# Performance work log

Measured on AMD Instinct MI355X. Metric: run time of the kernel, lower is better.

## Reference

```python
import jax, jax.numpy as jnp
import numpy as np

B, N, HN, HE, H = 8, 128, 256, 128, 8
DH = HN // H
P = N * (N - 1) // 2


def _ln(x, g, b, eps=1e-5):
    m = jnp.mean(x, axis=-1, keepdims=True)
    v = jnp.mean((x - m) ** 2, axis=-1, keepdims=True)
    return (x - m) * jax.lax.rsqrt(v + eps) * g + b


def setup_inputs() -> dict:
    key = jax.random.key(0)
    ks = jax.random.split(key, 16)
    i1, i2 = np.triu_indices(N, k=1)  # all unordered pairs, P = N(N-1)/2
    s = lambda fan: 1.0 / np.sqrt(fan)
    return {
        "node_feat": jax.random.normal(ks[0], (B, N, HN), jnp.float32),
        "edge_feat": jax.random.normal(ks[1], (B, P, HE), jnp.float32),
        "x_idx1": jnp.asarray(i1, jnp.int32),
        "x_idx2": jnp.asarray(i2, jnp.int32),
        "mask_valid": jax.random.bernoulli(ks[2], 0.9, (B, P)).astype(jnp.float32),
        "Wqkv": jax.random.normal(ks[3], (HN, 3 * HN), jnp.float32) * s(HN),
        "bqkv": jnp.zeros((3 * HN,), jnp.float32),
        "Wev": jax.random.normal(ks[4], (HE, HN), jnp.float32) * s(HE),
        "bev": jnp.zeros((HN,), jnp.float32),
        "Wea": jax.random.normal(ks[5], (HE, H), jnp.float32) * s(HE),
        "bea": jnp.zeros((H,), jnp.float32),
        "Wo": jax.random.normal(ks[6], (2 * HN, HN), jnp.float32) * s(2 * HN),
        "bo": jnp.zeros((HN,), jnp.float32),
        "Wsk": jax.random.normal(ks[7], (HN, 2 * HN), jnp.float32) * s(HN),
        "bsk": jnp.zeros((2 * HN,), jnp.float32),
        "gn": jnp.ones((HN,), jnp.float32),
        "bn": jnp.zeros((HN,), jnp.float32),
        "ge": jnp.ones((HE,), jnp.float32),
        "be": jnp.zeros((HE,), jnp.float32),
    }


def reference(node_feat, edge_feat, x_idx1, x_idx2, mask_valid,
              Wqkv, bqkv, Wev, bev, Wea, bea, Wo, bo, Wsk, bsk,
              gn, bn, ge, be):
    n_in = _ln(node_feat, gn, bn)                      # [B,N,HN]
    e_in = _ln(edge_feat, ge, be)                      # [B,P,HE]
    q, k, v = jnp.split(n_in @ Wqkv + bqkv, 3, axis=-1)
    to_h = lambda t: t.reshape(B, -1, H, DH).transpose(0, 2, 1, 3)
    q, k, v = to_h(q), to_h(k), to_h(v)                # [B,H,N,DH]
    e_val = to_h(e_in @ Wev + bev)                     # [B,H,P,DH]
    e_adj = (e_in @ Wea + bea).transpose(0, 2, 1)      # [B,H,P]

    scale = DH ** -0.5
    logits = jnp.einsum('bhqd,bhkd->bhqk', q, k) * scale  # [B,H,N,N]
    # per-pair logits; torch stacks [qk, edge_adj] then sums -> just add
    l_node1 = logits[:, :, x_idx1, x_idx2] + e_adj     # node i1 attends to i2
    l_node2 = logits[:, :, x_idx2, x_idx1] + e_adj     # node i2 attends to i1
    v_node1 = e_val + v[:, :, x_idx2]                  # value node i1 receives
    v_node2 = e_val + v[:, :, x_idx1]

    # group the 2P directed edges by destination node (= torch cat+sort+reshape)
    cat_idx = jnp.concatenate([x_idx1, x_idx2])        # [2P]
    order = jnp.argsort(cat_idx)                       # stable sort
    gl = jnp.concatenate([l_node1, l_node2], axis=2)[:, :, order].reshape(B, H, N, N - 1)
    gv = jnp.concatenate([v_node1, v_node2], axis=2)[:, :, order].reshape(B, H, N, N - 1, DH)
    gm = jnp.concatenate([mask_valid, mask_valid], axis=1)[:, order].reshape(B, N, N - 1)[:, None]  # [B,1,N,N-1]

    gl = jnp.where(gm == 0.0, -9e15, gl)
    probs = jax.nn.softmax(gl, axis=3)
    probs = probs * jnp.any(gm != 0.0, axis=3, keepdims=True).astype(probs.dtype)
    attn = jnp.einsum('bhnk,bhnkd->bhnd', probs, gv)   # [B,H,N,DH]
    attn = attn.transpose(0, 2, 1, 3).reshape(B, N, HN)

    comb = jax.nn.gelu(jnp.concatenate([n_in, attn], axis=-1) @ Wo + bo, approximate=False)
    val, gate = jnp.split(comb @ Wsk + bsk, 2, axis=-1)
    g = jax.nn.sigmoid(gate)
    return node_feat * (1.0 - g) + val * g
```

## Files before the change

kernel.cpp:

```cpp
#include <hip/hip_runtime.h>
#include <hip/hip_bf16.h>
#include <math.h>

#define BB 8
#define NN 128
#define HN 256
#define HE 128
#define NH 8
#define DH 32
#define PP 8128
#define BP (BB*PP)

typedef __hip_bfloat16 bf16;
typedef __hip_bfloat162 bf162;
typedef __attribute__((ext_vector_type(8))) short bf16x8;
typedef __attribute__((ext_vector_type(4))) float f32x4;

__device__ __forceinline__ float bf2f(bf16 x){ return __bfloat162float(x); }
__device__ __forceinline__ float bfraw2f(short u){
  return __uint_as_float(((unsigned)(unsigned short)u) << 16);
}

__device__ __forceinline__ float wave_sum(float v){
  #pragma unroll
  for (int off=32; off>=1; off>>=1) v += __shfl_xor(v, off, 64);
  return v;
}
__device__ __forceinline__ float wave_max(float v){
  #pragma unroll
  for (int off=32; off>=1; off>>=1) v = fmaxf(v, __shfl_xor(v, off, 64));
  return v;
}
__device__ __forceinline__ float g16_sum(float v){
  #pragma unroll
  for (int off=8; off>=1; off>>=1) v += __shfl_xor(v, off, 16);
  return v;
}

__device__ __forceinline__ int pair_idx(int a, int c){
  int i = a < c ? a : c;
  int j = a < c ? c : a;
  return ((i*(255 - i))>>1) + (j - i - 1);
}

#define C_NODE 0LL
#define C_MASK 262144LL
#define C_WQKV 327168LL
#define C_BQKV 523776LL
#define C_WEV  524544LL
#define C_BEV  557312LL
#define C_WEA  557568LL
#define C_BEA  558592LL
#define C_WO   558600LL
#define C_BO   689672LL
#define C_WSK  689928LL
#define C_BSK  821000LL
#define C_GN   821512LL
#define C_BN   821768LL
#define C_GE   822024LL
#define C_BE   822152LL
#define IOFF   822400LL
#define TOT8   102785
#define CONVBLKS 402
#define I_NIN  0LL
#define I_Q    262144LL
#define I_K    524288LL
#define I_V    786432LL
#define I_ATTN 1048576LL
#define I_COMB 1310720LL
#define I_EA2  1572864LL
#define I_XG   2093056LL
#define I_EVAL 6254592LL
#define I_WT   14577664LL
#define I_WOB  14594048LL
#define I_WSKB 14659584LL
#define I_FLG  14725120LL

struct SrcPtrs { const void* p[16]; };

__global__ __launch_bounds__(256) void k_convert(SrcPtrs sp, float* __restrict__ dst,
                                                 int* __restrict__ flags,
                                                 const unsigned short* __restrict__ nodeRaw,
                                                 const void* __restrict__ rawWev,
                                                 bf16* __restrict__ Wt,
                                                 const void* __restrict__ rawWo,
                                                 const void* __restrict__ rawWsk,
                                                 bf16* __restrict__ WoB,
                                                 bf16* __restrict__ WskB)
{
  __shared__ int sbad;
  if (threadIdx.x == 0) sbad = 0;
  __syncthreads();
  {
    int bad = 0;
    for (int i = threadIdx.x; i < 1024; i += 256){
      unsigned e = (nodeRaw[i] >> 7) & 0xFFu;
      if (e >= 194u) bad = 1;
    }
    if (bad) sbad = 1;
  }
  __syncthreads();
  const int f32 = sbad;
  if (blockIdx.x == 0 && threadIdx.x == 0) flags[0] = f32;

  if (blockIdx.x >= CONVBLKS + 128){
    int o = (blockIdx.x - (CONVBLKS + 128))*256 + threadIdx.x;
    const void* src = (o < 16384) ? rawWo : rawWsk;
    bf16* dw = (o < 16384) ? WoB : WskB;
    int lo = (o < 16384) ? o : o - 16384;
    if (f32){
      const float4* s4 = (const float4*)src;
      float4 a0 = s4[2*lo], a1 = s4[2*lo+1];
      union { float4 f; bf16 h[8]; } cv;
      cv.h[0]=__float2bfloat16(a0.x); cv.h[1]=__float2bfloat16(a0.y);
      cv.h[2]=__float2bfloat16(a0.z); cv.h[3]=__float2bfloat16(a0.w);
      cv.h[4]=__float2bfloat16(a1.x); cv.h[5]=__float2bfloat16(a1.y);
      cv.h[6]=__float2bfloat16(a1.z); cv.h[7]=__float2bfloat16(a1.w);
      *reinterpret_cast<float4*>(dw + lo*8) = cv.f;
    } else {
      *reinterpret_cast<float4*>(dw + lo*8) = ((const float4*)src)[lo];
    }
    return;
  }

  if (blockIdx.x >= CONVBLKS){
    int idx = (blockIdx.x - CONVBLKS)*256 + threadIdx.x;
    float v = f32 ? ((const float*)rawWev)[idx]
                  : bfraw2f(((const short*)rawWev)[idx]);
    Wt[(idx & 255)*128 + (idx >> 8)] = __float2bfloat16(v);
    return;
  }

  int o = blockIdx.x*256 + threadIdx.x;
  if (o >= TOT8) return;
  const int cum[17] = {0,32768,40896,65472,65568,69664,69696,69824,69825,
                       86209,86241,102625,102689,102721,102753,102769,102785};
  int s = 0;
  #pragma unroll
  for (int i = 1; i <= 15; i++) if (o >= cum[i]) s = i;
  const int li = o - cum[s];
  float4 r0, r1;
  if (f32){
    const float4* src = (const float4*)sp.p[s];
    r0 = src[2*li]; r1 = src[2*li+1];
  } else {
    union { float4 f; unsigned short u[8]; } cv;
    cv.f = ((const float4*)sp.p[s])[li];
    r0.x = __uint_as_float((unsigned)cv.u[0] << 16);
    r0.y = __uint_as_float((unsigned)cv.u[1] << 16);
    r0.z = __uint_as_float((unsigned)cv.u[2] << 16);
    r0.w = __uint_as_float((unsigned)cv.u[3] << 16);
    r1.x = __uint_as_float((unsigned)cv.u[4] << 16);
    r1.y = __uint_as_float((unsigned)cv.u[5] << 16);
    r1.z = __uint_as_float((unsigned)cv.u[6] << 16);
    r1.w = __uint_as_float((unsigned)cv.u[7] << 16);
  }
  float4* d = (float4*)(dst + (long long)cum[s]*8);
  d[2*li]   = r0;
  d[2*li+1] = r1;
}

__global__ __launch_bounds__(256) void k1_node_ln_qkv(
    const float* __restrict__ cnode, const float* __restrict__ cWqkv,
    const float* __restrict__ cbqkv, const float* __restrict__ cgn, const float* __restrict__ cbn,
    float* __restrict__ nin_ws, float* __restrict__ q_ws, float* __restrict__ k_ws,
    float* __restrict__ v_ws)
{
  __shared__ float xln[4][HN];
  const int t = threadIdx.x, wv = t>>6, lane = t&63;
  const int cb = blockIdx.x % 3;
  const int g0 = (blockIdx.x / 3) * 4;
  {
    int g = g0 + wv;
    float x[4];
    #pragma unroll
    for (int i=0;i<4;i++) x[i] = cnode[g*HN + lane + 64*i];
    float s = x[0]+x[1]+x[2]+x[3];
    s = wave_sum(s);
    float m = s * (1.0f/HN);
    float q = 0.f;
    #pragma unroll
    for (int i=0;i<4;i++){ float d = x[i]-m; q += d*d; }
    q = wave_sum(q);
    float rstd = rsqrtf(fmaxf(q*(1.0f/HN), 0.f) + 1e-5f);
    #pragma unroll
    for (int i=0;i<4;i++){
      int c = lane + 64*i;
      float y = (x[i]-m)*rstd*cgn[c] + cbn[c];
      xln[wv][c] = y;
      if (cb == 0) nin_ws[g*HN + c] = y;
    }
  }
  __syncthreads();
  const int col = cb*256 + t;
  float acc[4];
  {
    float bb = cbqkv[col];
    #pragma unroll
    for (int r=0;r<4;r++) acc[r] = bb;
  }
  for (int k=0;k<HN;k+=4){
    float4 xv[4];
    #pragma unroll
    for (int r=0;r<4;r++) xv[r] = *reinterpret_cast<const float4*>(&xln[r][k]);
    #pragma unroll
    for (int kk=0;kk<4;kk++){
      float w = cWqkv[(k+kk)*768 + col];
      #pragma unroll
      for (int r=0;r<4;r++) acc[r] = fmaf((&xv[r].x)[kk], w, acc[r]);
    }
  }
  float* dstp = (cb == 0) ? q_ws : (cb == 1) ? k_ws : v_ws;
  const int h = t>>5, d = t&31;
  #pragma unroll
  for (int r=0;r<4;r++){
    int g = g0 + r;
    int b = g>>7, n = g&127;
    dstp[((b*NH + h)*NN + n)*DH + d] = acc[r];
  }
}

__global__ __launch_bounds__(256) void k2a_edge_ln(
    const void* __restrict__ edge_raw, const float* __restrict__ cWea,
    const float* __restrict__ cbea, const float* __restrict__ cge,
    const float* __restrict__ cbe, const float* __restrict__ cmask,
    bf16* __restrict__ xg, float* __restrict__ ea2, const int* __restrict__ flags)
{
  __shared__ float xlnS[16][136];
  __shared__ float part[128];
  const int t = threadIdx.x;
  const int R0 = blockIdx.x*16;
  const int b = R0 / PP;
  const int p0 = R0 - b*PP;
  const int f32 = flags[0];
  {
    int r = t>>4, sub = t&15;
    long base = (long)(R0 + r)*HE + sub*8;
    float x[8];
    if (f32){
      const float* cef = (const float*)edge_raw + base;
      float4 a0 = *reinterpret_cast<const float4*>(cef);
      float4 a1 = *reinterpret_cast<const float4*>(cef + 4);
      x[0]=a0.x; x[1]=a0.y; x[2]=a0.z; x[3]=a0.w;
      x[4]=a1.x; x[5]=a1.y; x[6]=a1.z; x[7]=a1.w;
    } else {
      union { float4 f; short u[8]; } cv;
      cv.f = *reinterpret_cast<const float4*>((const bf16*)edge_raw + base);
      #pragma unroll
      for (int i=0;i<8;i++) x[i] = bfraw2f(cv.u[i]);
    }
    float s = 0.f;
    #pragma unroll
    for (int i=0;i<8;i++) s += x[i];
    s = g16_sum(s);
    float m = s*(1.0f/HE);
    float q = 0.f;
    #pragma unroll
    for (int i=0;i<8;i++){ float dd = x[i]-m; q += dd*dd; }
    q = g16_sum(q);
    float rstd = rsqrtf(fmaxf(q*(1.0f/HE), 0.f) + 1e-5f);
    #pragma unroll
    for (int i=0;i<8;i++){
      int c = sub*8 + i;
      xlnS[r][c] = (x[i]-m)*rstd*cge[c] + cbe[c];
    }
  }
  __syncthreads();
  {
    int r = t>>4, c0 = (t&15)*8;
    union { float4 f; bf16 h[8]; } o;
    #pragma unroll
    for (int i=0;i<8;i++) o.h[i] = __float2bfloat16(xlnS[r][c0+i]);
    *reinterpret_cast<float4*>(xg + (long)(R0 + r)*HE + c0) = o.f;
  }
  {
    const int c = t & 7, r = (t>>3) & 15, half = t>>7;
    const int pid = r*8 + c;
    float s = half ? 0.0f : cbea[c];
    const int k0 = half*64;
    #pragma unroll 8
    for (int k=k0; k<k0+64; k++) s = fmaf(xlnS[r][k], cWea[k*NH + c], s);
    if (half){ part[pid] = s; }
    __syncthreads();
    if (!half){
      s += part[pid];
      int p = p0 + r;
      float mk = cmask[b*PP + p];
      ea2[(b*NH + c)*PP + p] = (mk != 0.0f) ? s : -9e15f;
    }
  }
}

__global__ __launch_bounds__(256) void k2b_mfma(
    const bf16* __restrict__ xg, const bf16* __restrict__ Wt,
    const float* __restrict__ cbev, bf16* __restrict__ e_val)
{
  __shared__ bf16 Xs[64][136];
  __shared__ bf16 Ws[64][136];
  const int t = threadIdx.x;
  const int rowblk = blockIdx.x >> 2;
  const int cb = blockIdx.x & 3;
  const int b = rowblk / 127;
  const int p0 = (rowblk - b*127) * 64;
  const int n0 = cb * 64;
  #pragma unroll
  for (int it = 0; it < 4; ++it){
    int idx = it*256 + t;
    int r = idx >> 4, seg = idx & 15;
    float4 xv = *reinterpret_cast<const float4*>(xg + (long)(b*PP + p0 + r)*HE + seg*8);
    *reinterpret_cast<float4*>(&Xs[r][seg*8]) = xv;
    float4 wv = *reinterpret_cast<const float4*>(Wt + (long)(n0 + r)*HE + seg*8);
    *reinterpret_cast<float4*>(&Ws[r][seg*8]) = wv;
  }
  __syncthreads();
  const int wv = t>>6, lane = t&63;
  const int fm = lane & 15, q = lane >> 4;
  f32x4 acc[4];
  #pragma unroll
  for (int ct=0; ct<4; ++ct){
    float bb = cbev[n0 + ct*16 + fm];
    acc[ct][0]=bb; acc[ct][1]=bb; acc[ct][2]=bb; acc[ct][3]=bb;
  }
  #pragma unroll
  for (int ks=0; ks<4; ++ks){
    bf16x8 A = *reinterpret_cast<const bf16x8*>(&Xs[wv*16 + fm][ks*32 + q*8]);
    #pragma unroll
    for (int ct=0; ct<4; ++ct){
      bf16x8 Bf = *reinterpret_cast<const bf16x8*>(&Ws[ct*16 + fm][ks*32 + q*8]);
      acc[ct] = __builtin_amdgcn_mfma_f32_16x16x32_bf16(A, Bf, acc[ct], 0, 0, 0);
    }
  }
  #pragma unroll
  for (int ct=0; ct<4; ++ct){
    int col = n0 + ct*16 + fm;
    int h = col >> 5, d = col & 31;
    #pragma unroll
    for (int reg=0; reg<4; ++reg){
      int p = p0 + wv*16 + q*4 + reg;
      e_val[((long)(b*NH + h)*PP + p)*DH + d] = __float2bfloat16(acc[ct][reg]);
    }
  }
}

__global__ __launch_bounds__(256) void k3_attn(
    const float* __restrict__ q_ws, const float* __restrict__ k_ws, const float* __restrict__ v_ws,
    const bf16* __restrict__ e_val, const float* __restrict__ ea2,
    float* __restrict__ attn)
{
  __shared__ float kT[DH][NN+1];
  __shared__ float vS[NN][DH+1];
  __shared__ float qS[8][DH];
  __shared__ float pbuf[4][NN];
  const int t = threadIdx.x, wv = t>>6, lane = t&63;
  const int s16 = blockIdx.x & 15, h = (blockIdx.x>>4)&7, b = blockIdx.x>>7;
  const int bh = b*NH + h;
  const int n0 = s16*8;
  const float* kb = k_ws + (long)bh*NN*DH;
  const float* vb = v_ws + (long)bh*NN*DH;
  const float* qb = q_ws + ((long)bh*NN + n0)*DH;
  for (int idx=t; idx<NN*DH; idx+=256){
    int m = idx>>5, d = idx&31;
    kT[d][m] = kb[idx];
    vS[m][d] = vb[idx];
  }
  if (t < 8*DH) reinterpret_cast<float*>(qS)[t] = qb[t];
  __syncthreads();
  const float scale = 0.17677669529663687f;
  const float* eab = ea2 + (long)bh*PP;
  const bf16* evp = e_val + (long)bh*PP*DH;
  for (int it=0; it<2; ++it){
    const int nn = it*4 + wv;
    const int n = n0 + nn;
    const int m1 = lane, m2 = lane + 64;
    float dot1 = 0.f, dot2 = 0.f;
    #pragma unroll
    for (int d=0; d<DH; d++){
      float qd = qS[nn][d];
      dot1 = fmaf(qd, kT[d][m1], dot1);
      dot2 = fmaf(qd, kT[d][m2], dot2);
    }
    const bool self1 = (m1 == n), self2 = (m2 == n);
    int pr1 = pair_idx(n, self1 ? (m1^1) : m1);
    int pr2 = pair_idx(n, self2 ? (m2^1) : m2);
    float ea1 = eab[pr1], ea2v = eab[pr2];
    float l1 = self1 ? -INFINITY : dot1*scale + ea1;
    float l2 = self2 ? -INFINITY : dot2*scale + ea2v;
    bool av = (!self1 && ea1 > -8.9e15f) || (!self2 && ea2v > -8.9e15f);
    float lm = wave_max(fmaxf(l1, l2));
    float e1 = __expf(l1 - lm), e2 = __expf(l2 - lm);
    float ssum = wave_sum(e1 + e2);
    int anyv = __any((int)av);
    float inv = anyv ? (1.0f/ssum) : 0.0f;
    pbuf[wv][m1] = e1*inv;
    pbuf[wv][m2] = e2*inv;
    const int msub = lane & 15, oct = lane >> 4;
    float acc[8];
    #pragma unroll
    for (int e=0;e<8;e++) acc[e] = 0.f;
    #pragma unroll
    for (int mm=0; mm<128; mm+=16){
      int m = mm + msub;
      int ms = (m==n) ? (m^1) : m;
      int pr = pair_idx(n, ms);
      bf16x8 ev8 = *reinterpret_cast<const bf16x8*>(evp + (long)pr*DH + oct*8);
      float pm = pbuf[wv][m];
      const float* vrow = &vS[m][oct*8];
      #pragma unroll
      for (int e=0;e<8;e++){
        acc[e] = fmaf(pm, vrow[e] + bfraw2f(ev8[e]), acc[e]);
      }
    }
    #pragma unroll
    for (int off=1; off<16; off<<=1){
      #pragma unroll
      for (int e=0;e<8;e++) acc[e] += __shfl_xor(acc[e], off, 64);
    }
    if (msub == 0){
      float* op = attn + ((long)b*NN + n)*HN + h*DH + oct*8;
      float4 o0 = {acc[0],acc[1],acc[2],acc[3]};
      float4 o1 = {acc[4],acc[5],acc[6],acc[7]};
      *reinterpret_cast<float4*>(op) = o0;
      *reinterpret_cast<float4*>(op+4) = o1;
    }
  }
}

__global__ __launch_bounds__(256) void k4_wo_gelu(
    const float* __restrict__ nin_ws, const float* __restrict__ attn,
    const bf16* __restrict__ WoB, const float* __restrict__ cbo,
    float* __restrict__ comb)
{
  __shared__ float xc[4][512];
  __shared__ float ps[3][4][64];
  const int t = threadIdx.x;
  const int g0 = (blockIdx.x >> 2) * 4;
  const int cq = blockIdx.x & 3;
  {
    int r = t>>6, c0 = (t&63)*8;
    const float* src = (c0 < 256) ? (nin_ws + (long)(g0+r)*HN + c0)
                                  : (attn + (long)(g0+r)*HN + (c0-256));
    float4 a0 = *reinterpret_cast<const float4*>(src);
    float4 a1 = *reinterpret_cast<const float4*>(src+4);
    *reinterpret_cast<float4*>(&xc[r][c0]) = a0;
    *reinterpret_cast<float4*>(&xc[r][c0+4]) = a1;
  }
  __syncthreads();
  const int cidx = t & 63, ks = t >> 6;
  const int col = cq*64 + cidx;
  float acc[4] = {0.f,0.f,0.f,0.f};
  const int k0 = ks*128;
  #pragma unroll 4
  for (int k=k0; k<k0+128; k++){
    float w = bf2f(WoB[k*HN + col]);
    #pragma unroll
    for (int r=0;r<4;r++) acc[r] = fmaf(xc[r][k], w, acc[r]);
  }
  if (ks){
    #pragma unroll
    for (int r=0;r<4;r++) ps[ks-1][r][cidx] = acc[r];
  }
  __syncthreads();
  if (!ks){
    float bb = cbo[col];
    #pragma unroll
    for (int r=0;r<4;r++){
      float x = acc[r] + bb + ps[0][r][cidx] + ps[1][r][cidx] + ps[2][r][cidx];
      comb[(long)(g0+r)*HN + col] = 0.5f*x*(1.0f + erff(x*0.7071067811865475f));
    }
  }
}

__global__ __launch_bounds__(256) void k5_sk_gate(
    const float* __restrict__ comb, const float* __restrict__ cnode,
    const bf16* __restrict__ WskB, const float* __restrict__ cbsk,
    void* __restrict__ out, const int* __restrict__ flags)
{
  __shared__ float xc[4][HN];
  __shared__ float psv[3][4][64];
  __shared__ float psg[3][4][64];
  const int t = threadIdx.x;
  const int g0 = (blockIdx.x >> 2) * 4;
  const int cq = blockIdx.x & 3;
  {
    int r = t>>6, c0 = (t&63)*4;
    *reinterpret_cast<float4*>(&xc[r][c0]) =
        *reinterpret_cast<const float4*>(comb + (long)(g0+r)*HN + c0);
  }
  __syncthreads();
  const int cidx = t & 63, ks = t >> 6;
  const int col = cq*64 + cidx;
  float av[4] = {0.f,0.f,0.f,0.f}, ag[4] = {0.f,0.f,0.f,0.f};
  const int k0 = ks*64;
  #pragma unroll 4
  for (int k=k0; k<k0+64; k++){
    float wv = bf2f(WskB[k*512 + col]);
    float wg = bf2f(WskB[k*512 + col + 256]);
    #pragma unroll
    for (int r=0;r<4;r++){
      float xr = xc[r][k];
      av[r] = fmaf(xr, wv, av[r]);
      ag[r] = fmaf(xr, wg, ag[r]);
    }
  }
  if (ks){
    #pragma unroll
    for (int r=0;r<4;r++){ psv[ks-1][r][cidx] = av[r]; psg[ks-1][r][cidx] = ag[r]; }
  }
  __syncthreads();
  if (!ks){
    const int f32 = flags[0];
    float bv = cbsk[col], bg = cbsk[col+256];
    #pragma unroll
    for (int r=0;r<4;r++){
      float v = av[r] + bv + psv[0][r][cidx] + psv[1][r][cidx] + psv[2][r][cidx];
      float g = ag[r] + bg + psg[0][r][cidx] + psg[1][r][cidx] + psg[2][r][cidx];
      float gg = 1.0f/(1.0f + __expf(-g));
      float nf = cnode[(long)(g0+r)*HN + col];
      float res = nf*(1.0f - gg) + v*gg;
      if (f32) ((float*)out)[(long)(g0+r)*HN + col] = res;
      else ((bf16*)out)[(long)(g0+r)*HN + col] = __float2bfloat16(res);
    }
  }
}

extern "C" void kernel_launch(void* const* d_in, const int* in_sizes, int n_inputs,
                              void* d_out, int out_size, void* d_ws, size_t ws_size,
                              hipStream_t stream)
{
  float* ws = (float*)d_ws;
  float* c_node = ws + C_NODE;
  float* c_mask = ws + C_MASK;
  float* c_Wqkv = ws + C_WQKV;
  float* c_bqkv = ws + C_BQKV;
  float* c_bev  = ws + C_BEV;
  float* c_Wea  = ws + C_WEA;
  float* c_bea  = ws + C_BEA;
  float* c_bo   = ws + C_BO;
  float* c_bsk  = ws + C_BSK;
  float* c_gn   = ws + C_GN;
  float* c_bn   = ws + C_BN;
  float* c_ge   = ws + C_GE;
  float* c_be   = ws + C_BE;
  float* base   = ws + IOFF;
  float* nin_ws  = base + I_NIN;
  float* q_ws    = base + I_Q;
  float* k_ws    = base + I_K;
  float* v_ws    = base + I_V;
  float* attn_ws = base + I_ATTN;
  float* comb_ws = base + I_COMB;
  float* ea2_ws  = base + I_EA2;
  bf16*  xg_ws   = (bf16*)(base + I_XG);
  bf16*  eval_ws = (bf16*)(base + I_EVAL);
  bf16*  wt_ws   = (bf16*)(base + I_WT);
  bf16*  wob_ws  = (bf16*)(base + I_WOB);
  bf16*  wskb_ws = (bf16*)(base + I_WSKB);
  int*   flags   = (int*)(base + I_FLG);

  SrcPtrs sp;
  sp.p[0]  = d_in[0];
  sp.p[1]  = d_in[4];
  sp.p[2]  = d_in[5];
  sp.p[3]  = d_in[6];
  sp.p[4]  = d_in[7];
  sp.p[5]  = d_in[8];
  sp.p[6]  = d_in[9];
  sp.p[7]  = d_in[10];
  sp.p[8]  = d_in[11];
  sp.p[9]  = d_in[12];
  sp.p[10] = d_in[13];
  sp.p[11] = d_in[14];
  sp.p[12] = d_in[15];
  sp.p[13] = d_in[16];
  sp.p[14] = d_in[17];
  sp.p[15] = d_in[18];

  k_convert<<<CONVBLKS + 256, 256, 0, stream>>>(sp, ws, flags,
                                                (const unsigned short*)d_in[0],
                                                d_in[7], wt_ws,
                                                d_in[11], d_in[13],
                                                wob_ws, wskb_ws);
  k1_node_ln_qkv<<<768, 256, 0, stream>>>(c_node, c_Wqkv, c_bqkv, c_gn, c_bn,
                                          nin_ws, q_ws, k_ws, v_ws);
  k2a_edge_ln<<<BP/16, 256, 0, stream>>>(d_in[1], c_Wea, c_bea, c_ge, c_be, c_mask,
                                         xg_ws, ea2_ws, flags);
  k2b_mfma<<<4064, 256, 0, stream>>>(xg_ws, wt_ws, c_bev, eval_ws);
  k3_attn<<<BB*NH*16, 256, 0, stream>>>(q_ws, k_ws, v_ws, eval_ws, ea2_ws, attn_ws);
  k4_wo_gelu<<<1024, 256, 0, stream>>>(nin_ws, attn_ws, wob_ws, c_bo, comb_ws);
  k5_sk_gate<<<1024, 256, 0, stream>>>(comb_ws, c_node, wskb_ws, c_bsk, d_out, flags);
}
```

Before: 200.2 us.

## Fold edge-value projection after attention aggregation, dropping e_val materialization

Removes the separate MFMA kernel that computed and stored per-pair edge values (B*H*P*DH bf16). Because the projection is linear, the attention kernel now aggregates the normalized edge features with the attention probabilities and then applies Wev once per node and head, adding the bias scaled by the any-valid flag. Attention is reorganized to one block per (batch, node) covering all heads, with ea2 and v re-laid out so the per-pair reads are contiguous. This cuts a large intermediate write and read. In exchange each block gathers 128 rows of edge features and each thread runs a small scalar GEMV.

Result: slower. 238.0 us (+18.9%).

```diff
diff --git a/kernel.cpp b/kernel.cpp
--- a/kernel.cpp
+++ b/kernel.cpp
@@ -24,11 +24,6 @@
 __device__ __forceinline__ float wave_sum(float v){
   #pragma unroll
   for (int off=32; off>=1; off>>=1) v += __shfl_xor(v, off, 64);
-  return v;
-}
-__device__ __forceinline__ float wave_max(float v){
-  #pragma unroll
-  for (int off=32; off>=1; off>>=1) v = fmaxf(v, __shfl_xor(v, off, 64));
   return v;
 }
 __device__ __forceinline__ float g16_sum(float v){
@@ -70,7 +65,6 @@
 #define I_COMB 1310720LL
 #define I_EA2  1572864LL
 #define I_XG   2093056LL
-#define I_EVAL 6254592LL
 #define I_WT   14577664LL
 #define I_WOB  14594048LL
 #define I_WSKB 14659584LL
@@ -210,13 +204,18 @@
       for (int r=0;r<4;r++) acc[r] = fmaf((&xv[r].x)[kk], w, acc[r]);
     }
   }
-  float* dstp = (cb == 0) ? q_ws : (cb == 1) ? k_ws : v_ws;
-  const int h = t>>5, d = t&31;
-  #pragma unroll
-  for (int r=0;r<4;r++){
-    int g = g0 + r;
-    int b = g>>7, n = g&127;
-    dstp[((b*NH + h)*NN + n)*DH + d] = acc[r];
+  if (cb == 2){
+    #pragma unroll
+    for (int r=0;r<4;r++) v_ws[(long)(g0+r)*HN + t] = acc[r];
+  } else {
+    float* dstp = (cb == 0) ? q_ws : k_ws;
+    const int h = t>>5, d = t&31;
+    #pragma unroll
+    for (int r=0;r<4;r++){
+      int g = g0 + r;
+      int b = g>>7, n = g&127;
+      dstp[((b*NH + h)*NN + n)*DH + d] = acc[r];
+    }
   }
 }
 
@@ -286,143 +285,134 @@
       s += part[pid];
       int p = p0 + r;
       float mk = cmask[b*PP + p];
-      ea2[(b*NH + c)*PP + p] = (mk != 0.0f) ? s : -9e15f;
-    }
-  }
-}
-
-__global__ __launch_bounds__(256) void k2b_mfma(
-    const bf16* __restrict__ xg, const bf16* __restrict__ Wt,
-    const float* __restrict__ cbev, bf16* __restrict__ e_val)
-{
-  __shared__ bf16 Xs[64][136];
-  __shared__ bf16 Ws[64][136];
+      ea2[((long)b*PP + p)*8 + c] = (mk != 0.0f) ? s : -9e15f;
+    }
+  }
+}
+
+__global__ __launch_bounds__(256) void k3_attn(
+    const float* __restrict__ q_ws,
+    const float* __restrict__ k_ws,
+    const float* __restrict__ v_ws,
+    const bf16* __restrict__ xg,
+    const float* __restrict__ ea2,
+    const bf16* __restrict__ Wt,
+    const float* __restrict__ cbev,
+    float* __restrict__ attn)
+{
+  __shared__ __align__(16) float qS[8][32];
+  __shared__ __align__(16) int   prS[128];
+  __shared__ __align__(16) float eaS[128][8];
+  __shared__ __align__(16) float pS[8][128];
+  __shared__ __align__(16) float sS[8][128];
+  __shared__ float anyS[8];
   const int t = threadIdx.x;
-  const int rowblk = blockIdx.x >> 2;
-  const int cb = blockIdx.x & 3;
-  const int b = rowblk / 127;
-  const int p0 = (rowblk - b*127) * 64;
-  const int n0 = cb * 64;
-  #pragma unroll
-  for (int it = 0; it < 4; ++it){
-    int idx = it*256 + t;
-    int r = idx >> 4, seg = idx & 15;
-    float4 xv = *reinterpret_cast<const float4*>(xg + (long)(b*PP + p0 + r)*HE + seg*8);
-    *reinterpret_cast<float4*>(&Xs[r][seg*8]) = xv;
-    float4 wv = *reinterpret_cast<const float4*>(Wt + (long)(n0 + r)*HE + seg*8);
-    *reinterpret_cast<float4*>(&Ws[r][seg*8]) = wv;
-  }
-  __syncthreads();
-  const int wv = t>>6, lane = t&63;
-  const int fm = lane & 15, q = lane >> 4;
-  f32x4 acc[4];
-  #pragma unroll
-  for (int ct=0; ct<4; ++ct){
-    float bb = cbev[n0 + ct*16 + fm];
-    acc[ct][0]=bb; acc[ct][1]=bb; acc[ct][2]=bb; acc[ct][3]=bb;
-  }
-  #pragma unroll
-  for (int ks=0; ks<4; ++ks){
-    bf16x8 A = *reinterpret_cast<const bf16x8*>(&Xs[wv*16 + fm][ks*32 + q*8]);
-    #pragma unroll
-    for (int ct=0; ct<4; ++ct){
-      bf16x8 Bf = *reinterpret_cast<const bf16x8*>(&Ws[ct*16 + fm][ks*32 + q*8]);
-      acc[ct] = __builtin_amdgcn_mfma_f32_16x16x32_bf16(A, Bf, acc[ct], 0, 0, 0);
-    }
-  }
-  #pragma unroll
-  for (int ct=0; ct<4; ++ct){
-    int col = n0 + ct*16 + fm;
-    int h = col >> 5, d = col & 31;
-    #pragma unroll
-    for (int reg=0; reg<4; ++reg){
-      int p = p0 + wv*16 + q*4 + reg;
-      e_val[((long)(b*NH + h)*PP + p)*DH + d] = __float2bfloat16(acc[ct][reg]);
-    }
-  }
-}
-
-__global__ __launch_bounds__(256) void k3_attn(
-    const float* __restrict__ q_ws, const float* __restrict__ k_ws, const float* __restrict__ v_ws,
-    const bf16* __restrict__ e_val, const float* __restrict__ ea2,
-    float* __restrict__ attn)
-{
-  __shared__ float kT[DH][NN+1];
-  __shared__ float vS[NN][DH+1];
-  __shared__ float qS[8][DH];
-  __shared__ float pbuf[4][NN];
-  const int t = threadIdx.x, wv = t>>6, lane = t&63;
-  const int s16 = blockIdx.x & 15, h = (blockIdx.x>>4)&7, b = blockIdx.x>>7;
-  const int bh = b*NH + h;
-  const int n0 = s16*8;
-  const float* kb = k_ws + (long)bh*NN*DH;
-  const float* vb = v_ws + (long)bh*NN*DH;
-  const float* qb = q_ws + ((long)bh*NN + n0)*DH;
-  for (int idx=t; idx<NN*DH; idx+=256){
-    int m = idx>>5, d = idx&31;
-    kT[d][m] = kb[idx];
-    vS[m][d] = vb[idx];
-  }
-  if (t < 8*DH) reinterpret_cast<float*>(qS)[t] = qb[t];
-  __syncthreads();
+  const int bid = blockIdx.x;
+  const int swz = (bid & 7)*128 + (bid >> 3);
+  const int n = swz & 127, b = swz >> 7;
+  const int h = t >> 5, ln = t & 31;
+
+  qS[h][ln] = q_ws[(((long)b*NH + h)*NN + n)*DH + ln];
+  if (t < 128){
+    int m = t;
+    prS[m] = pair_idx(n, (m == n) ? (m ^ 1) : m);
+  }
+  __syncthreads();
+  {
+    int m = t >> 1, c0 = (t & 1)*4;
+    float4 ev = *reinterpret_cast<const float4*>(ea2 + ((long)b*PP + prS[m])*8 + c0);
+    *reinterpret_cast<float4*>(&eaS[m][c0]) = ev;
+  }
+  __syncthreads();
+
   const float scale = 0.17677669529663687f;
-  const float* eab = ea2 + (long)bh*PP;
-  const bf16* evp = e_val + (long)bh*PP*DH;
-  for (int it=0; it<2; ++it){
-    const int nn = it*4 + wv;
-    const int n = n0 + nn;
-    const int m1 = lane, m2 = lane + 64;
-    float dot1 = 0.f, dot2 = 0.f;
-    #pragma unroll
-    for (int d=0; d<DH; d++){
-      float qd = qS[nn][d];
-      dot1 = fmaf(qd, kT[d][m1], dot1);
-      dot2 = fmaf(qd, kT[d][m2], dot2);
-    }
-    const bool self1 = (m1 == n), self2 = (m2 == n);
-    int pr1 = pair_idx(n, self1 ? (m1^1) : m1);
-    int pr2 = pair_idx(n, self2 ? (m2^1) : m2);
-    float ea1 = eab[pr1], ea2v = eab[pr2];
-    float l1 = self1 ? -INFINITY : dot1*scale + ea1;
-    float l2 = self2 ? -INFINITY : dot2*scale + ea2v;
-    bool av = (!self1 && ea1 > -8.9e15f) || (!self2 && ea2v > -8.9e15f);
-    float lm = wave_max(fmaxf(l1, l2));
-    float e1 = __expf(l1 - lm), e2 = __expf(l2 - lm);
-    float ssum = wave_sum(e1 + e2);
-    int anyv = __any((int)av);
-    float inv = anyv ? (1.0f/ssum) : 0.0f;
-    pbuf[wv][m1] = e1*inv;
-    pbuf[wv][m2] = e2*inv;
-    const int msub = lane & 15, oct = lane >> 4;
-    float acc[8];
-    #pragma unroll
-    for (int e=0;e<8;e++) acc[e] = 0.f;
-    #pragma unroll
-    for (int mm=0; mm<128; mm+=16){
-      int m = mm + msub;
-      int ms = (m==n) ? (m^1) : m;
-      int pr = pair_idx(n, ms);
-      bf16x8 ev8 = *reinterpret_cast<const bf16x8*>(evp + (long)pr*DH + oct*8);
-      float pm = pbuf[wv][m];
-      const float* vrow = &vS[m][oct*8];
-      #pragma unroll
-      for (int e=0;e<8;e++){
-        acc[e] = fmaf(pm, vrow[e] + bfraw2f(ev8[e]), acc[e]);
+  float4 qv[8];
+  #pragma unroll
+  for (int d4=0; d4<8; d4++) qv[d4] = *reinterpret_cast<const float4*>(&qS[h][d4*4]);
+  const float* kb = k_ws + ((long)b*NH + h)*NN*DH;
+  float l[4];
+  float mx = -INFINITY;
+  int valid = 0;
+  #pragma unroll
+  for (int j=0;j<4;j++){
+    int m = ln + 32*j;
+    const float* kr = kb + m*DH;
+    float dot = 0.f;
+    #pragma unroll
+    for (int d4=0; d4<8; d4++){
+      float4 kv = *reinterpret_cast<const float4*>(kr + d4*4);
+      dot = fmaf((&qv[d4].x)[0], kv.x, dot);
+      dot = fmaf((&qv[d4].x)[1], kv.y, dot);
+      dot = fmaf((&qv[d4].x)[2], kv.z, dot);
+      dot = fmaf((&qv[d4].x)[3], kv.w, dot);
+    }
+    float eav = eaS[m][h];
+    bool self = (m == n);
+    l[j] = self ? -INFINITY : fmaf(dot, scale, eav);
+    if (!self && eav > -8.9e15f) valid = 1;
+    mx = fmaxf(mx, l[j]);
+  }
+  #pragma unroll
+  for (int off=16; off>=1; off>>=1) mx = fmaxf(mx, __shfl_xor(mx, off, 32));
+  float e[4], s = 0.f;
+  #pragma unroll
+  for (int j=0;j<4;j++){ e[j] = __expf(l[j]-mx); s += e[j]; }
+  float av = valid ? 1.f : 0.f;
+  #pragma unroll
+  for (int off=16; off>=1; off>>=1){
+    s  += __shfl_xor(s,  off, 32);
+    av += __shfl_xor(av, off, 32);
+  }
+  float inv = (av > 0.f) ? (1.0f/s) : 0.f;
+  #pragma unroll
+  for (int j=0;j<4;j++) pS[h][ln+32*j] = e[j]*inv;
+  if (ln == 0) anyS[h] = (av > 0.f) ? 1.f : 0.f;
+  __syncthreads();
+
+  const bf16* xgb = xg + (long)b*PP*HE;
+  const float* vb = v_ws + (long)b*NN*HN + h*DH + ln;
+  float S0=0.f,S1=0.f,S2=0.f,S3=0.f,T=0.f;
+  for (int m0=0; m0<128; m0+=4){
+    float4 p4 = *reinterpret_cast<const float4*>(&pS[h][m0]);
+    int4  pr4 = *reinterpret_cast<const int4*>(&prS[m0]);
+    #pragma unroll
+    for (int i=0;i<4;i++){
+      float pm = (&p4.x)[i];
+      if (pm != 0.f){
+        int pr = (&pr4.x)[i];
+        short4 xv = *reinterpret_cast<const short4*>(
+            reinterpret_cast<const short*>(xgb + (long)pr*HE) + ln*4);
+        S0 = fmaf(pm, bfraw2f(xv.x), S0);
+        S1 = fmaf(pm, bfraw2f(xv.y), S1);
+        S2 = fmaf(pm, bfraw2f(xv.z), S2);
+        S3 = fmaf(pm, bfraw2f(xv.w), S3);
+        T  = fmaf(pm, vb[(m0+i)*HN], T);
       }
     }
-    #pragma unroll
-    for (int off=1; off<16; off<<=1){
-      #pragma unroll
-      for (int e=0;e<8;e++) acc[e] += __shfl_xor(acc[e], off, 64);
-    }
-    if (msub == 0){
-      float* op = attn + ((long)b*NN + n)*HN + h*DH + oct*8;
-      float4 o0 = {acc[0],acc[1],acc[2],acc[3]};
-      float4 o1 = {acc[4],acc[5],acc[6],acc[7]};
-      *reinterpret_cast<float4*>(op) = o0;
-      *reinterpret_cast<float4*>(op+4) = o1;
-    }
-  }
+  }
+  {
+    float4 sv; sv.x=S0; sv.y=S1; sv.z=S2; sv.w=S3;
+    *reinterpret_cast<float4*>(&sS[h][ln*4]) = sv;
+  }
+  __syncthreads();
+
+  float acc = T + anyS[h]*cbev[h*DH + ln];
+  const bf16* wr = Wt + (h*DH + ln)*HE;
+  #pragma unroll 4
+  for (int k0=0;k0<128;k0+=8){
+    float4 sa = *reinterpret_cast<const float4*>(&sS[h][k0]);
+    float4 sb = *reinterpret_cast<const float4*>(&sS[h][k0+4]);
+    bf16x8 wv = *reinterpret_cast<const bf16x8*>(wr + k0);
+    acc = fmaf(sa.x, bfraw2f(wv[0]), acc);
+    acc = fmaf(sa.y, bfraw2f(wv[1]), acc);
+    acc = fmaf(sa.z, bfraw2f(wv[2]), acc);
+    acc = fmaf(sa.w, bfraw2f(wv[3]), acc);
+    acc = fmaf(sb.x, bfraw2f(wv[4]), acc);
+    acc = fmaf(sb.y, bfraw2f(wv[5]), acc);
+    acc = fmaf(sb.z, bfraw2f(wv[6]), acc);
+    acc = fmaf(sb.w, bfraw2f(wv[7]), acc);
+  }
+  attn[((long)b*NN + n)*HN + h*DH + ln] = acc;
 }
 
 __global__ __launch_bounds__(256) void k4_wo_gelu(
@@ -550,7 +540,6 @@
   float* comb_ws = base + I_COMB;
   float* ea2_ws  = base + I_EA2;
   bf16*  xg_ws   = (bf16*)(base + I_XG);
-  bf16*  eval_ws = (bf16*)(base + I_EVAL);
   bf16*  wt_ws   = (bf16*)(base + I_WT);
   bf16*  wob_ws  = (bf16*)(base + I_WOB);
   bf16*  wskb_ws = (bf16*)(base + I_WSKB);
@@ -583,8 +572,8 @@
                                           nin_ws, q_ws, k_ws, v_ws);
   k2a_edge_ln<<<BP/16, 256, 0, stream>>>(d_in[1], c_Wea, c_bea, c_ge, c_be, c_mask,
                                          xg_ws, ea2_ws, flags);
-  k2b_mfma<<<4064, 256, 0, stream>>>(xg_ws, wt_ws, c_bev, eval_ws);
-  k3_attn<<<BB*NH*16, 256, 0, stream>>>(q_ws, k_ws, v_ws, eval_ws, ea2_ws, attn_ws);
+  k3_attn<<<BB*NN, 256, 0, stream>>>(q_ws, k_ws, v_ws, xg_ws, ea2_ws, wt_ws, c_bev,
+                                     attn_ws);
   k4_wo_gelu<<<1024, 256, 0, stream>>>(nin_ws, attn_ws, wob_ws, c_bo, comb_ws);
   k5_sk_gate<<<1024, 256, 0, stream>>>(comb_ws, c_node, wskb_ws, c_bsk, d_out, flags);
 }
```
